# Optimization experiments

Measured on AMD Instinct MI355X. Metric: run time of the kernel, lower is better.

Reference implementation:

```python
import jax, jax.numpy as jnp
import numpy as np
import math

N = 4096
BATCH = 8192


def _bitrev_perm(n):
    stages = int(math.log2(n))
    idx = np.arange(n, dtype=np.int64)
    rev = np.zeros(n, dtype=np.int64)
    v = idx.copy()
    for _ in range(stages):
        rev = (rev << 1) | (v & 1)
        v >>= 1
    return rev


def setup_inputs() -> dict:
    key = jax.random.key(0)
    k1, k2 = jax.random.split(key)
    x_re = jax.random.normal(k1, (BATCH, N), dtype=jnp.float32)
    x_im = jax.random.normal(k2, (BATCH, N), dtype=jnp.float32)
    k = np.arange(N, dtype=np.float32)
    angles = -2.0 * np.pi * k / N
    W_re = jnp.asarray(np.cos(angles), dtype=jnp.float32)
    W_im = jnp.asarray(np.sin(angles), dtype=jnp.float32)
    bitrev = jnp.asarray(_bitrev_perm(N))
    return {"x_re": x_re, "x_im": x_im, "W_re": W_re, "W_im": W_im, "bitrev": bitrev}


def reference(x_re, x_im, W_re, W_im, bitrev):
    n = x_re.shape[-1]
    num_stages = int(math.log2(n))
    # bit-reversal input permutation (the "wiring")
    y_re = x_re[..., bitrev]
    y_im = x_im[..., bitrev]
    for stage in range(num_stages):
        stride = 1 << stage
        group_size = stride << 1
        num_groups = n // group_size
        # (..., num_groups, group_size)
        y_re = y_re.reshape(*y_re.shape[:-1], num_groups, group_size)
        y_im = y_im.reshape(*y_im.shape[:-1], num_groups, group_size)
        upper_re = y_re[..., :stride]
        upper_im = y_im[..., :stride]
        lower_re = y_re[..., stride:]
        lower_im = y_im[..., stride:]
        tw_step = n // group_size
        tw_idx = jnp.arange(stride) * tw_step
        Wr = W_re[tw_idx]
        Wi = W_im[tw_idx]
        # complex twiddle multiply: W * lower
        wb_re = Wr * lower_re - Wi * lower_im
        wb_im = Wr * lower_im + Wi * lower_re
        y_re = jnp.concatenate([upper_re + wb_re, upper_re - wb_re], axis=-1)
        y_im = jnp.concatenate([upper_im + wb_im, upper_im - wb_im], axis=-1)
        y_re = y_re.reshape(*y_re.shape[:-2], n)
        y_im = y_im.reshape(*y_im.shape[:-2], n)
    return (y_re, y_im)
```

## Files before the change

### kernel.cpp

```cpp
#include <hip/hip_runtime.h>

#define FFT_N   4096
#define THREADS 512

__device__ __forceinline__ float2 cmul(float2 w, float2 v) {
    return make_float2(fmaf(w.x, v.x, -w.y * v.y), fmaf(w.x, v.y, w.y * v.x));
}
__device__ __forceinline__ float2 cmni(float2 v) { return make_float2(v.y, -v.x); }
__device__ __forceinline__ void bfly(float2& a, float2& b, float2 w) {
    float2 t = cmul(w, b);
    b = make_float2(a.x - t.x, a.y - t.y);
    a = make_float2(a.x + t.x, a.y + t.y);
}
__device__ __forceinline__ int swz(int i) { return i ^ ((i >> 4) & 15) ^ ((i >> 8) & 15); }

__device__ __forceinline__ void bar() {
    asm volatile("s_waitcnt lgkmcnt(0)" ::: "memory");
    __builtin_amdgcn_s_barrier();
}
__device__ __forceinline__ void radix8(float2 u[8], float2 A, float2 B, float2 C, float2 D) {
    bfly(u[0], u[1], A); bfly(u[2], u[3], A); bfly(u[4], u[5], A); bfly(u[6], u[7], A);
    float2 Bn = cmni(B);
    bfly(u[0], u[2], B); bfly(u[1], u[3], Bn); bfly(u[4], u[6], B); bfly(u[5], u[7], Bn);
    float2 Cn = cmni(C), Dn = cmni(D);
    bfly(u[0], u[4], C); bfly(u[1], u[5], D); bfly(u[2], u[6], Cn); bfly(u[3], u[7], Dn);
}

struct Row { float2 u[8]; };

__device__ __forceinline__ void load_row(Row& r, const float* __restrict__ xr,
                                         const float* __restrict__ xi, int t) {
    const int off[8] = {0, 2048, 1024, 3072, 512, 2560, 1536, 3584};
#pragma unroll
    for (int j = 0; j < 8; ++j) r.u[j] = make_float2(xr[t + off[j]], xi[t + off[j]]);
}

__device__ __forceinline__ void issue2(Row& n, int a, int b, int offa, int offb,
                                       const float* __restrict__ xr,
                                       const float* __restrict__ xi, int t, bool en) {
    if (en) {
        n.u[a] = make_float2(xr[t + offa], xi[t + offa]);
        n.u[b] = make_float2(xr[t + offb], xi[t + offb]);
    }
    asm volatile("" ::: "memory");
}

__device__ __forceinline__ void process_row(Row& r, float2* lds, int t,
        float2 C1, float2 C2, float2 C3, float2 w512,
        float* __restrict__ yr, float* __restrict__ yi,
        Row& nxt, const float* __restrict__ nxr, const float* __restrict__ nxi, bool en)
{
    const float2 one = make_float2(1.f, 0.f);

    issue2(nxt, 0, 1, 0, 2048, nxr, nxi, t, en);
    radix8(r.u, one, one, one, w512);
    const int g0 = (int)(__brev((unsigned)t) >> 23);
#pragma unroll
    for (int j = 0; j < 8; ++j) lds[swz(8 * g0 + j)] = r.u[j];
    bar();

    issue2(nxt, 2, 3, 1024, 3072, nxr, nxi, t, en);
    const int b1 = (t & 7) | (((t >> 4) & 1) << 6) | (((t >> 3) & 1) << 7) | ((t >> 5) << 8);
#pragma unroll
    for (int j = 0; j < 8; ++j) r.u[j] = lds[swz(b1 + 8 * j)];
    { float2 B = cmul(C1, C1), A = cmul(B, B), D = cmul(C1, w512);
      radix8(r.u, A, B, C1, D); }
#pragma unroll
    for (int j = 0; j < 8; ++j) lds[swz(b1 + 8 * j)] = r.u[j];
    bar();

    issue2(nxt, 4, 5, 512, 2560, nxr, nxi, t, en);
    const int b2 = (t & 63) | ((t >> 6) << 9);
#pragma unroll
    for (int j = 0; j < 8; ++j) r.u[j] = lds[swz(b2 + 64 * j)];
    { float2 B = cmul(C2, C2), A = cmul(B, B), D = cmul(C2, w512);
      radix8(r.u, A, B, C2, D); }
#pragma unroll
    for (int j = 0; j < 8; ++j) lds[swz(b2 + 64 * j)] = r.u[j];
    bar();

    issue2(nxt, 6, 7, 1536, 3584, nxr, nxi, t, en);
#pragma unroll
    for (int j = 0; j < 8; ++j) r.u[j] = lds[swz(t + 512 * j)];
    { float2 B = cmul(C3, C3), A = cmul(B, B), D = cmul(C3, w512);
      radix8(r.u, A, B, C3, D); }
#pragma unroll
    for (int j = 0; j < 8; ++j) { yr[t + 512 * j] = r.u[j].x; yi[t + 512 * j] = r.u[j].y; }
    bar();
}

__global__ __launch_bounds__(THREADS) void fft4096_pin_kernel(
    const float* __restrict__ x_re, const float* __restrict__ x_im,
    const float* __restrict__ W_re, const float* __restrict__ W_im,
    float* __restrict__ out, int batch, int rows_per)
{
    __shared__ float2 lds[FFT_N];
    const int t = threadIdx.x;

    const float2 C1 = make_float2(W_re[(t & 7) << 6],  W_im[(t & 7) << 6]);
    const float2 C2 = make_float2(W_re[(t & 63) << 3], W_im[(t & 63) << 3]);
    const float2 C3 = make_float2(W_re[t],             W_im[t]);
    const float2 w512 = make_float2(0.70710678118654752f, -0.70710678118654752f);

    const int row0 = blockIdx.x * rows_per;
    Row A, B;

    if (rows_per & 1) {
        for (int i = 0; i < rows_per; ++i) {
            const int r = row0 + i;
            load_row(A, x_re + (size_t)r * FFT_N, x_im + (size_t)r * FFT_N, t);
            asm volatile("" ::: "memory");
            process_row(A, lds, t, C1, C2, C3, w512,
                        out + (size_t)r * FFT_N, out + ((size_t)batch + r) * FFT_N,
                        B, x_re, x_im, false);
        }
        return;
    }

    load_row(A, x_re + (size_t)row0 * FFT_N, x_im + (size_t)row0 * FFT_N, t);
    asm volatile("" ::: "memory");
    for (int i = 0; i < rows_per; i += 2) {
        const int r0 = row0 + i, r1 = r0 + 1;
        const bool en2 = (i + 2) < rows_per;
        const int r2 = en2 ? (r0 + 2) : row0;
        process_row(A, lds, t, C1, C2, C3, w512,
                    out + (size_t)r0 * FFT_N, out + ((size_t)batch + r0) * FFT_N,
                    B, x_re + (size_t)r1 * FFT_N, x_im + (size_t)r1 * FFT_N, true);
        process_row(B, lds, t, C1, C2, C3, w512,
                    out + (size_t)r1 * FFT_N, out + ((size_t)batch + r1) * FFT_N,
                    A, x_re + (size_t)r2 * FFT_N, x_im + (size_t)r2 * FFT_N, en2);
    }
}

extern "C" void kernel_launch(void* const* d_in, const int* in_sizes, int n_in,
                              void* d_out, int out_size, void* d_ws, size_t ws_size,
                              hipStream_t stream) {
    const float* x_re = (const float*)d_in[0];
    const float* x_im = (const float*)d_in[1];
    const float* W_re = (const float*)d_in[2];
    const float* W_im = (const float*)d_in[3];
    const int batch = in_sizes[0] / FFT_N;
    float* out = (float*)d_out;

    int rows_per = 8;
    while (rows_per > 1 && (batch % rows_per)) rows_per >>= 1;
    const int grid = batch / rows_per;
    fft4096_pin_kernel<<<grid, THREADS, 0, stream>>>(x_re, x_im, W_re, W_im, out, batch, rows_per);
}
```

Before: 112.0 us.

## Skew two rows across double LDS buffers to halve barriers per row

Splits the per-row FFT into four pass functions and interleaves two rows in a software pipeline. Each row gets its own LDS buffer, and passes of row A and row B share a barrier, which cuts the number of barriers per row and gives the scheduler independent work inside each phase. Rows per block drop from 8 to 4 and launch bounds now request 4 blocks per CU. The cost is 64 KB of LDS per block, which caps occupancy, plus extra register pressure from holding two rows' data at once.

```diff
diff --git a/kernel.cpp b/kernel.cpp
--- a/kernel.cpp
+++ b/kernel.cpp
@@ -1,7 +1,8 @@
 #include <hip/hip_runtime.h>
 
-#define FFT_N   4096
-#define THREADS 512
+#define FFT_N    4096
+#define THREADS  512
+#define ROWS_PER 4
 
 __device__ __forceinline__ float2 cmul(float2 w, float2 v) {
     return make_float2(fmaf(w.x, v.x, -w.y * v.y), fmaf(w.x, v.y, w.y * v.x));
@@ -35,66 +36,62 @@
     for (int j = 0; j < 8; ++j) r.u[j] = make_float2(xr[t + off[j]], xi[t + off[j]]);
 }
 
-__device__ __forceinline__ void issue2(Row& n, int a, int b, int offa, int offb,
-                                       const float* __restrict__ xr,
+template <int J0>
+__device__ __forceinline__ void issue4(Row& n, const float* __restrict__ xr,
                                        const float* __restrict__ xi, int t, bool en) {
+    const int off[8] = {0, 2048, 1024, 3072, 512, 2560, 1536, 3584};
     if (en) {
-        n.u[a] = make_float2(xr[t + offa], xi[t + offa]);
-        n.u[b] = make_float2(xr[t + offb], xi[t + offb]);
+#pragma unroll
+        for (int j = J0; j < J0 + 4; ++j) n.u[j] = make_float2(xr[t + off[j]], xi[t + off[j]]);
     }
     asm volatile("" ::: "memory");
 }
 
-__device__ __forceinline__ void process_row(Row& r, float2* lds, int t,
-        float2 C1, float2 C2, float2 C3, float2 w512,
-        float* __restrict__ yr, float* __restrict__ yi,
-        Row& nxt, const float* __restrict__ nxr, const float* __restrict__ nxi, bool en)
-{
+__device__ __forceinline__ void passP0(Row& r, float2* lds, int t, float2 w512) {
     const float2 one = make_float2(1.f, 0.f);
-
-    issue2(nxt, 0, 1, 0, 2048, nxr, nxi, t, en);
     radix8(r.u, one, one, one, w512);
     const int g0 = (int)(__brev((unsigned)t) >> 23);
 #pragma unroll
     for (int j = 0; j < 8; ++j) lds[swz(8 * g0 + j)] = r.u[j];
-    bar();
-
-    issue2(nxt, 2, 3, 1024, 3072, nxr, nxi, t, en);
+}
+__device__ __forceinline__ void passP1(float2* lds, int t, float2 C1, float2 w512) {
+    Row s;
     const int b1 = (t & 7) | (((t >> 4) & 1) << 6) | (((t >> 3) & 1) << 7) | ((t >> 5) << 8);
 #pragma unroll
-    for (int j = 0; j < 8; ++j) r.u[j] = lds[swz(b1 + 8 * j)];
-    { float2 B = cmul(C1, C1), A = cmul(B, B), D = cmul(C1, w512);
-      radix8(r.u, A, B, C1, D); }
+    for (int j = 0; j < 8; ++j) s.u[j] = lds[swz(b1 + 8 * j)];
+    float2 B = cmul(C1, C1), A = cmul(B, B), D = cmul(C1, w512);
+    radix8(s.u, A, B, C1, D);
 #pragma unroll
-    for (int j = 0; j < 8; ++j) lds[swz(b1 + 8 * j)] = r.u[j];
-    bar();
-
-    issue2(nxt, 4, 5, 512, 2560, nxr, nxi, t, en);
+    for (int j = 0; j < 8; ++j) lds[swz(b1 + 8 * j)] = s.u[j];
+}
+__device__ __forceinline__ void passP2(float2* lds, int t, float2 C2, float2 w512) {
+    Row s;
     const int b2 = (t & 63) | ((t >> 6) << 9);
 #pragma unroll
-    for (int j = 0; j < 8; ++j) r.u[j] = lds[swz(b2 + 64 * j)];
-    { float2 B = cmul(C2, C2), A = cmul(B, B), D = cmul(C2, w512);
-      radix8(r.u, A, B, C2, D); }
+    for (int j = 0; j < 8; ++j) s.u[j] = lds[swz(b2 + 64 * j)];
+    float2 B = cmul(C2, C2), A = cmul(B, B), D = cmul(C2, w512);
+    radix8(s.u, A, B, C2, D);
 #pragma unroll
-    for (int j = 0; j < 8; ++j) lds[swz(b2 + 64 * j)] = r.u[j];
-    bar();
-
-    issue2(nxt, 6, 7, 1536, 3584, nxr, nxi, t, en);
+    for (int j = 0; j < 8; ++j) lds[swz(b2 + 64 * j)] = s.u[j];
+}
+__device__ __forceinline__ void passP3(float2* lds, int t, float2 C3, float2 w512,
+                                       float* __restrict__ yr, float* __restrict__ yi) {
+    Row s;
 #pragma unroll
-    for (int j = 0; j < 8; ++j) r.u[j] = lds[swz(t + 512 * j)];
-    { float2 B = cmul(C3, C3), A = cmul(B, B), D = cmul(C3, w512);
-      radix8(r.u, A, B, C3, D); }
+    for (int j = 0; j < 8; ++j) s.u[j] = lds[swz(t + 512 * j)];
+    float2 B = cmul(C3, C3), A = cmul(B, B), D = cmul(C3, w512);
+    radix8(s.u, A, B, C3, D);
 #pragma unroll
-    for (int j = 0; j < 8; ++j) { yr[t + 512 * j] = r.u[j].x; yi[t + 512 * j] = r.u[j].y; }
-    bar();
+    for (int j = 0; j < 8; ++j) { yr[t + 512 * j] = s.u[j].x; yi[t + 512 * j] = s.u[j].y; }
 }
 
-__global__ __launch_bounds__(THREADS) void fft4096_pin_kernel(
+__global__ __launch_bounds__(THREADS, 4) void fft4096_skew_kernel(
     const float* __restrict__ x_re, const float* __restrict__ x_im,
     const float* __restrict__ W_re, const float* __restrict__ W_im,
     float* __restrict__ out, int batch, int rows_per)
 {
-    __shared__ float2 lds[FFT_N];
+    __shared__ float2 L0[FFT_N];
+    __shared__ float2 L1[FFT_N];
     const int t = threadIdx.x;
 
     const float2 C1 = make_float2(W_re[(t & 7) << 6],  W_im[(t & 7) << 6]);
@@ -102,34 +99,67 @@
     const float2 C3 = make_float2(W_re[t],             W_im[t]);
     const float2 w512 = make_float2(0.70710678118654752f, -0.70710678118654752f);
 
-    const int row0 = blockIdx.x * rows_per;
-    Row A, B;
+    const int base = blockIdx.x * rows_per;
+    float* out_im = out + (size_t)batch * FFT_N;
+    Row X, Y;
 
     if (rows_per & 1) {
         for (int i = 0; i < rows_per; ++i) {
-            const int r = row0 + i;
-            load_row(A, x_re + (size_t)r * FFT_N, x_im + (size_t)r * FFT_N, t);
+            const int r = base + i;
+            load_row(X, x_re + (size_t)r * FFT_N, x_im + (size_t)r * FFT_N, t);
             asm volatile("" ::: "memory");
-            process_row(A, lds, t, C1, C2, C3, w512,
-                        out + (size_t)r * FFT_N, out + ((size_t)batch + r) * FFT_N,
-                        B, x_re, x_im, false);
+            passP0(X, L0, t, w512);                                   bar();
+            passP1(L0, t, C1, w512);                                  bar();
+            passP2(L0, t, C2, w512);                                  bar();
+            passP3(L0, t, C3, w512, out + (size_t)r * FFT_N, out_im + (size_t)r * FFT_N);
+            bar();
         }
         return;
     }
 
-    load_row(A, x_re + (size_t)row0 * FFT_N, x_im + (size_t)row0 * FFT_N, t);
+    load_row(X, x_re + (size_t)base * FFT_N, x_im + (size_t)base * FFT_N, t);
     asm volatile("" ::: "memory");
-    for (int i = 0; i < rows_per; i += 2) {
-        const int r0 = row0 + i, r1 = r0 + 1;
-        const bool en2 = (i + 2) < rows_per;
-        const int r2 = en2 ? (r0 + 2) : row0;
-        process_row(A, lds, t, C1, C2, C3, w512,
-                    out + (size_t)r0 * FFT_N, out + ((size_t)batch + r0) * FFT_N,
-                    B, x_re + (size_t)r1 * FFT_N, x_im + (size_t)r1 * FFT_N, true);
-        process_row(B, lds, t, C1, C2, C3, w512,
-                    out + (size_t)r1 * FFT_N, out + ((size_t)batch + r1) * FFT_N,
-                    A, x_re + (size_t)r2 * FFT_N, x_im + (size_t)r2 * FFT_N, en2);
+
+    bool hp = false;
+    int prevB = 0;
+    for (int it = 0; it < rows_per / 2; ++it) {
+        const int a = base + 2 * it, b = a + 1;
+        const bool more = (it + 1) < rows_per / 2;
+        const int a2 = more ? (a + 2) : base;
+        const float* bxr = x_re + (size_t)b * FFT_N;
+        const float* bxi = x_im + (size_t)b * FFT_N;
+        const float* cxr = x_re + (size_t)a2 * FFT_N;
+        const float* cxi = x_im + (size_t)a2 * FFT_N;
+
+        issue4<0>(Y, bxr, bxi, t, true);
+        passP0(X, L0, t, w512);
+        if (hp) passP2(L1, t, C2, w512);
+        bar();
+
+        issue4<4>(Y, bxr, bxi, t, true);
+        if (hp) passP3(L1, t, C3, w512,
+                       out + (size_t)prevB * FFT_N, out_im + (size_t)prevB * FFT_N);
+        passP1(L0, t, C1, w512);
+        bar();
+
+        issue4<0>(X, cxr, cxi, t, more);
+        passP0(Y, L1, t, w512);
+        passP2(L0, t, C2, w512);
+        bar();
+
+        issue4<4>(X, cxr, cxi, t, more);
+        passP3(L0, t, C3, w512,
+               out + (size_t)a * FFT_N, out_im + (size_t)a * FFT_N);
+        passP1(L1, t, C1, w512);
+        bar();
+
+        hp = true; prevB = b;
     }
+
+    passP2(L1, t, C2, w512);
+    bar();
+    passP3(L1, t, C3, w512,
+           out + (size_t)prevB * FFT_N, out_im + (size_t)prevB * FFT_N);
 }
 
 extern "C" void kernel_launch(void* const* d_in, const int* in_sizes, int n_in,
@@ -142,8 +172,8 @@
     const int batch = in_sizes[0] / FFT_N;
     float* out = (float*)d_out;
 
-    int rows_per = 8;
+    int rows_per = ROWS_PER;
     while (rows_per > 1 && (batch % rows_per)) rows_per >>= 1;
     const int grid = batch / rows_per;
-    fft4096_pin_kernel<<<grid, THREADS, 0, stream>>>(x_re, x_im, W_re, W_im, out, batch, rows_per);
+    fft4096_skew_kernel<<<grid, THREADS, 0, stream>>>(x_re, x_im, W_re, W_im, out, batch, rows_per);
 }
```

After: 249.0 us. 2.22x slower.
